# Kernel optimization log

Measured on AMD Instinct MI355X. Metric: run time of the kernel, lower is better.

## Reference

```python
import jax, jax.numpy as jnp
import numpy as np

NUM_LEVELS = 4
RADIUS = 4


def _bilinear_zeros(img, x, y):
    """Bilinear sample img (N,H,W) at absolute pixel coords x,y (N,S,S),
    zeros padding outside, matching torch grid_sample(align_corners=True,
    padding_mode='zeros') with absolute->normalized->absolute roundtrip."""
    N, H, W = img.shape
    x0 = jnp.floor(x); y0 = jnp.floor(y)
    x1 = x0 + 1.0;     y1 = y0 + 1.0
    wx1 = x - x0; wx0 = 1.0 - wx1
    wy1 = y - y0; wy0 = 1.0 - wy1
    flat = img.reshape(N, H * W)

    def gather(xi, yi):
        valid = (xi >= 0) & (xi <= W - 1) & (yi >= 0) & (yi <= H - 1)
        xc = jnp.clip(xi, 0, W - 1).astype(jnp.int32)
        yc = jnp.clip(yi, 0, H - 1).astype(jnp.int32)
        idx = (yc * W + xc).reshape(N, -1)
        v = jnp.take_along_axis(flat, idx, axis=1).reshape(xi.shape)
        return jnp.where(valid, v, jnp.zeros((), img.dtype))

    return (wy0 * wx0 * gather(x0, y0) + wy0 * wx1 * gather(x1, y0)
            + wy1 * wx0 * gather(x0, y1) + wy1 * wx1 * gather(x1, y1))


def _avg_pool2(v):
    N, H, W = v.shape
    return v.reshape(N, H // 2, 2, W // 2, 2).mean(axis=(2, 4))


def setup_inputs() -> dict:
    key = jax.random.key(0)
    k1, k2, k3 = jax.random.split(key, 3)
    B, M, C, H, W = 2, 4096, 256, 64, 64
    fmap1 = jax.random.normal(k1, (B, M, C), dtype=jnp.float32)
    fmap2 = jax.random.normal(k2, (B, C, H, W), dtype=jnp.float32)
    u = jax.random.uniform(k3, (B, M, 2), dtype=jnp.float32)
    centroids_coords = u * jnp.array([W - 1, H - 1], dtype=jnp.float32)
    return {"fmap1": fmap1, "fmap2": fmap2, "centroids_coords": centroids_coords}


def reference(fmap1, fmap2, centroids_coords):
    B, M, C = fmap1.shape
    _, _, H, W = fmap2.shape
    side = 2 * RADIUS + 1

    # correlation volume: (B, M, H, W) -> (B*M, H, W)
    corr = jnp.einsum('bmc,bchw->bmhw', fmap1, fmap2).reshape(B * M, H, W)

    d = jnp.arange(-RADIUS, RADIUS + 1, dtype=centroids_coords.dtype)
    di, dj = jnp.meshgrid(d, d, indexing='ij')
    delta = jnp.stack([di, dj], axis=-1)  # (S, S, 2): ch0 = x-offset, ch1 = y-offset

    c = centroids_coords.reshape(B * M, 1, 1, 2)
    vol = corr
    feats = []
    for lvl in range(NUM_LEVELS):
        sc = c + delta                        # (B*M, S, S, 2)
        sampled = _bilinear_zeros(vol, sc[..., 0], sc[..., 1])
        feats.append(sampled.reshape(B, M, side * side))
        c = c / 2.0
        if lvl < NUM_LEVELS - 1:
            vol = _avg_pool2(vol)
    # (B, M, num_levels*S*S) -> (B, out_channels, M)
    return jnp.concatenate(feats, axis=-1).transpose(0, 2, 1)
```

## Files before the change

### kernel.cpp

```cpp
#include <hip/hip_runtime.h>
#include <stdint.h>
#include <stddef.h>

static constexpr int Bb = 2;
static constexpr int Mq = 4096;
static constexpr int Cc = 256;
static constexpr int Hh = 64, Ww = 64;
static constexpr int Np = Hh * Ww;
static constexpr int NL1 = 1024;
static constexpr int RAD = 4;
static constexpr int SIDE = 2 * RAD + 1;
static constexpr int KPL = SIDE * SIDE;
static constexpr int NLVL = 4;
static constexpr int KTOT = NLVL * KPL;

static constexpr size_t L1BUF_B  = 0;
static constexpr size_t WINBUF_B = (size_t)Bb * Mq * 1024 * 2;
static constexpr size_t ABF_B    = WINBUF_B + (size_t)Bb * Mq * 100 * 4;
static constexpr size_t BT_B     = ABF_B + (size_t)Bb * Mq * Cc * 2;
static constexpr size_t B1T_B    = BT_B + (size_t)Bb * Np * Cc * 2;

typedef float floatx4 __attribute__((ext_vector_type(4)));
typedef short shortx8 __attribute__((ext_vector_type(8)));

union BfPack {
    shortx8 v;
    unsigned short u[8];
};

__device__ __forceinline__ unsigned short f2bf(float f) {
    unsigned int x = __float_as_uint(f);
    x += 0x7fffu + ((x >> 16) & 1u);
    return (unsigned short)(x >> 16);
}

__device__ __forceinline__ float bf2f(unsigned short u) {
    return __uint_as_float((unsigned int)u << 16);
}

__device__ __forceinline__ void gll16(const void* g, void* l) {
    __builtin_amdgcn_global_load_lds(
        (const __attribute__((address_space(1))) unsigned int*)g,
        (__attribute__((address_space(3))) unsigned int*)l, 16, 0, 0);
}

__global__ __launch_bounds__(256)
void cvt_kernel(const float* __restrict__ f1, const float* __restrict__ f2,
                unsigned short* __restrict__ Abf, unsigned short* __restrict__ Bt,
                unsigned short* __restrict__ B1t)
{
    __shared__ float tile[64 * 132];
    const int tid = threadIdx.x;
    if (blockIdx.x < 1024) {
        const int t = blockIdx.x * 256 + tid;
        const float4 v0 = *(const float4*)(f1 + (size_t)t * 8);
        const float4 v1 = *(const float4*)(f1 + (size_t)t * 8 + 4);
        BfPack p;
        p.u[0] = f2bf(v0.x); p.u[1] = f2bf(v0.y);
        p.u[2] = f2bf(v0.z); p.u[3] = f2bf(v0.w);
        p.u[4] = f2bf(v1.x); p.u[5] = f2bf(v1.y);
        p.u[6] = f2bf(v1.z); p.u[7] = f2bf(v1.w);
        *(shortx8*)(Abf + (size_t)t * 8) = p.v;
        return;
    }
    const int bid  = blockIdx.x - 1024;
    const int b    = bid >> 7;
    const int cblk = (bid >> 5) & 3;
    const int y1   = bid & 31;

#pragma unroll
    for (int i = 0; i < 8; ++i) {
        const int v  = i * 256 + tid;
        const int c  = v >> 5;
        const int f4 = v & 31;
        *(float4*)&tile[c * 132 + f4 * 4] =
            *(const float4*)&f2[((size_t)(b * Cc + cblk * 64 + c)) * Np + y1 * 128 + f4 * 4];
    }
    __syncthreads();

#pragma unroll
    for (int i = 0; i < 4; ++i) {
        const int w  = i * 256 + tid;
        const int rp = w >> 3;
        const int cg = w & 7;
        BfPack p;
#pragma unroll
        for (int u = 0; u < 8; ++u)
            p.u[u] = f2bf(tile[(cg * 8 + u) * 132 + rp]);
        *(shortx8*)&Bt[((size_t)(b * Np + y1 * 128 + rp)) * Cc + cblk * 64 + cg * 8] = p.v;
    }

    {
        const int x1 = tid >> 3;
        const int cg = tid & 7;
        BfPack p;
#pragma unroll
        for (int u = 0; u < 8; ++u) {
            const int c = cg * 8 + u;
            const float v = 0.25f * (tile[c * 132 + 2 * x1]      + tile[c * 132 + 2 * x1 + 1]
                                   + tile[c * 132 + 64 + 2 * x1] + tile[c * 132 + 64 + 2 * x1 + 1]);
            p.u[u] = f2bf(v);
        }
        *(shortx8*)&B1t[((size_t)(b * NL1 + y1 * 32 + x1)) * Cc + cblk * 64 + cg * 8] = p.v;
    }
}

__global__ __launch_bounds__(512)
void win_kernel(const unsigned short* __restrict__ Abf,
                const unsigned short* __restrict__ Bt,
                const float* __restrict__ cent,
                float* __restrict__ winbuf)
{
    __shared__ unsigned short reg[176 * 264];
    __shared__ int qlist[128];
    __shared__ int qx0s[128], qy0s[128];
    __shared__ int qcnt;

    const int tid  = threadIdx.x;
    const int b    = blockIdx.x >> 8;
    const int cell = blockIdx.x & 255;
    const int biny = cell >> 4;
    const int binx = cell & 15;
    const int xmin = (4 * binx - 4) > 0 ? (4 * binx - 4) : 0;
    const int ymin = (4 * biny - 4) > 0 ? (4 * biny - 4) : 0;
    const int xmax = (4 * binx + 8) < 63 ? (4 * binx + 8) : 63;
    const int ymax = (4 * biny + 8) < 63 ? (4 * biny + 8) : 63;
    const int rh = ymax - ymin + 1;
    const int rw = xmax - xmin + 1;

    if (tid == 0) qcnt = 0;
    __syncthreads();

#pragma unroll
    for (int i = 0; i < 8; ++i) {
        const int m = i * 512 + tid;
        const float2 cc = *(const float2*)&cent[((size_t)b * Mq + m) * 2];
        const int fx = (int)floorf(cc.x);
        const int fy = (int)floorf(cc.y);
        if ((fx >> 2) == binx && (fy >> 2) == biny) {
            const int idx = atomicAdd(&qcnt, 1);
            if (idx < 128) {
                qlist[idx] = m;
                qx0s[idx] = fx - RAD;
                qy0s[idx] = fy - RAD;
            }
        }
    }

    for (int ry = 0; ry < rh; ++ry) {
        const size_t gbase = ((size_t)(b * Np) + (size_t)((ymin + ry) * Ww + xmin)) * Cc;
        const int nchunk = rw * 32;
        if (tid < nchunk) {
            const int px = tid >> 5;
            const int g  = tid & 31;
            *(shortx8*)&reg[(ry * 13 + px) * 264 + g * 8] =
                *(const shortx8*)&Bt[gbase + (size_t)tid * 8];
        }
    }
    __syncthreads();

    const int cnt = qcnt < 128 ? qcnt : 128;
    const int wave   = tid >> 6;
    const int lane   = tid & 63;
    const int lane15 = lane & 15;
    const int quad   = lane >> 4;

    for (int m0 = 0; m0 < cnt; m0 += 16) {
        const int qidx = (m0 + lane15) < cnt ? (m0 + lane15) : (cnt - 1);
        const unsigned short* arow =
            Abf + (size_t)(b * Mq + qlist[qidx]) * Cc + quad * 8;
        shortx8 afr[8];
#pragma unroll
        for (int k0 = 0; k0 < 8; ++k0)
            afr[k0] = *(const shortx8*)&arow[k0 * 32];

        const int jt0 = wave, jt1 = wave + 8;
        floatx4 acc0 = {0.f, 0.f, 0.f, 0.f};
        floatx4 acc1 = {0.f, 0.f, 0.f, 0.f};
#pragma unroll
        for (int k0 = 0; k0 < 8; ++k0) {
            const shortx8 b0 =
                *(const shortx8*)&reg[(jt0 * 16 + lane15) * 264 + k0 * 32 + quad * 8];
            acc0 = __builtin_amdgcn_mfma_f32_16x16x32_bf16(afr[k0], b0, acc0, 0, 0, 0);
            if (wave < 3) {
                const shortx8 b1 =
                    *(const shortx8*)&reg[(jt1 * 16 + lane15) * 264 + k0 * 32 + quad * 8];
                acc1 = __builtin_amdgcn_mfma_f32_16x16x32_bf16(afr[k0], b1, acc1, 0, 0, 0);
            }
        }

#pragma unroll
        for (int t = 0; t < 2; ++t) {
            if (t == 1 && wave >= 3) break;
            const int jt = (t == 0) ? jt0 : jt1;
            const floatx4 a = (t == 0) ? acc0 : acc1;
            const int col = jt * 16 + lane15;
            const int py = col / 13;
            const int px = col - py * 13;
            if (py < rh && px < rw) {
                const int y = ymin + py, x = xmin + px;
#pragma unroll
                for (int r = 0; r < 4; ++r) {
                    const int qi = m0 + quad * 4 + r;
                    if (qi < cnt) {
                        const int wy = y - qy0s[qi];
                        const int wx = x - qx0s[qi];
                        if ((unsigned)wy < 10u && (unsigned)wx < 10u)
                            winbuf[((size_t)b * Mq + qlist[qi]) * 100 + wy * 10 + wx] = a[r];
                    }
                }
            }
        }
    }
}

__global__ __launch_bounds__(256)
void l1_gemm_kernel(const unsigned short* __restrict__ Abf,
                    const unsigned short* __restrict__ B1t,
                    unsigned short* __restrict__ l1buf)
{
    __shared__ union {
        unsigned short stage[2][2][128 * 32];
        float corrT[32 * 132];
    } sm;

    const int b    = blockIdx.z;
    const int bm0  = blockIdx.y * 128;
    const int bn0  = blockIdx.x * 128;
    const int tid  = threadIdx.x;
    const int lane = tid & 63;
    const int wave = tid >> 6;
    const int lane15 = lane & 15;
    const int quad   = lane >> 4;
    const int wm = (wave >> 1) * 64;
    const int wn = (wave & 1) * 64;

    const int lrow = lane >> 2;
    const int lkg  = (((lane & 3) ^ ((lrow >> 1) & 3))) * 8;
    const unsigned short* aptr = Abf + (size_t)(b * Mq + bm0 + wave * 16 + lrow) * Cc + lkg;
    const unsigned short* bptr = B1t + (size_t)(b * NL1 + bn0 + wave * 16 + lrow) * Cc + lkg;

    floatx4 acc[4][4];
#pragma unroll
    for (int i = 0; i < 4; ++i)
#pragma unroll
        for (int j = 0; j < 4; ++j)
            acc[i][j] = floatx4{0.0f, 0.0f, 0.0f, 0.0f};

    gll16(aptr,           &sm.stage[0][0][wave * 512]);
    gll16(aptr + 64 * Cc, &sm.stage[0][0][2048 + wave * 512]);
    gll16(bptr,           &sm.stage[0][1][wave * 512]);
    gll16(bptr + 64 * Cc, &sm.stage[0][1][2048 + wave * 512]);

    const int rq = (quad ^ ((lane15 >> 1) & 3)) * 8;

    for (int k0 = 0; k0 < 8; ++k0) {
        __syncthreads();
        if (k0 < 7) {
            const int nb = (k0 + 1) & 1;
            const int ko = (k0 + 1) * 32;
            gll16(aptr + ko,           &sm.stage[nb][0][wave * 512]);
            gll16(aptr + 64 * Cc + ko, &sm.stage[nb][0][2048 + wave * 512]);
            gll16(bptr + ko,           &sm.stage[nb][1][wave * 512]);
            gll16(bptr + 64 * Cc + ko, &sm.stage[nb][1][2048 + wave * 512]);
        }
        const unsigned short* la = sm.stage[k0 & 1][0];
        const unsigned short* lb = sm.stage[k0 & 1][1];
        shortx8 af[4], bf[4];
#pragma unroll
        for (int i = 0; i < 4; ++i)
            af[i] = *(const shortx8*)&la[(wm + i * 16 + lane15) * 32 + rq];
#pragma unroll
        for (int j = 0; j < 4; ++j)
            bf[j] = *(const shortx8*)&lb[(wn + j * 16 + lane15) * 32 + rq];
#pragma unroll
        for (int i = 0; i < 4; ++i)
#pragma unroll
            for (int j = 0; j < 4; ++j)
                acc[i][j] = __builtin_amdgcn_mfma_f32_16x16x32_bf16(
                    af[i], bf[j], acc[i][j], 0, 0, 0);
    }

    float* corrT = sm.corrT;
    const int row = tid >> 3;
    const int g   = tid & 7;
#pragma unroll
    for (int c = 0; c < 4; ++c) {
        __syncthreads();
        if ((wave >> 1) == (c >> 1)) {
#pragma unroll
            for (int ii = 0; ii < 2; ++ii) {
                const int i = 2 * (c & 1) + ii;
#pragma unroll
                for (int j = 0; j < 4; ++j) {
#pragma unroll
                    for (int reg = 0; reg < 4; ++reg) {
                        const int rl = ii * 16 + quad * 4 + reg;
                        const int n  = wn + j * 16 + lane15;
                        corrT[rl * 132 + n] = acc[i][j][reg];
                    }
                }
            }
        }
        __syncthreads();

        const size_t gq = (size_t)(b * Mq + bm0 + 32 * c + row);
        const float* T = &corrT[row * 132];
        BfPack p0, p1;
#pragma unroll
        for (int u = 0; u < 8; ++u) {
            p0.u[u] = f2bf(T[g * 16 + u]);
            p1.u[u] = f2bf(T[g * 16 + 8 + u]);
        }
        *(shortx8*)&l1buf[gq * 1024 + bn0 + g * 16]     = p0.v;
        *(shortx8*)&l1buf[gq * 1024 + bn0 + g * 16 + 8] = p1.v;
    }
}

__global__ __launch_bounds__(256)
void pyr_sample_kernel(const float* __restrict__ cent,
                       const unsigned short* __restrict__ l1buf,
                       const float* __restrict__ winbuf,
                       float* __restrict__ out)
{
    __shared__ float l1[8][1024];
    __shared__ float l2[8][256];
    __shared__ float l3[8][64];
    __shared__ float win0[8][100];
    __shared__ float qcx[8], qcy[8];
    __shared__ int   qx0[8], qy0[8];

    const int tid = threadIdx.x;
    const int b   = blockIdx.x >> 9;
    const int m0  = (blockIdx.x & 511) * 8;
    const size_t gq0 = (size_t)(b * Mq + m0);

    if (tid < 8) {
        const float cx = cent[(gq0 + tid) * 2 + 0];
        const float cy = cent[(gq0 + tid) * 2 + 1];
        qcx[tid] = cx; qcy[tid] = cy;
        qx0[tid] = (int)floorf(cx) - RAD;
        qy0[tid] = (int)floorf(cy) - RAD;
    }

#pragma unroll
    for (int it = 0; it < 4; ++it) {
        const int v = it * 256 + tid;
        const int q = v >> 7;
        const int o = v & 127;
        BfPack p;
        p.v = *(const shortx8*)&l1buf[(gq0 + q) * 1024 + o * 8];
#pragma unroll
        for (int u = 0; u < 8; ++u)
            l1[q][o * 8 + u] = bf2f(p.u[u]);
    }
    if (tid < 200) {
        const int q = tid / 25;
        const int o = tid - q * 25;
        *(float4*)&win0[q][o * 4] = *(const float4*)&winbuf[(gq0 + q) * 100 + o * 4];
    }
    __syncthreads();

#pragma unroll
    for (int i = 0; i < 8; ++i) {
        const int idx = i * 256 + tid;
        const int q = idx >> 8;
        const int c = idx & 255;
        const int cy2 = c >> 4, cx2 = c & 15;
        const float* s = &l1[q][(2 * cy2) * 32 + 2 * cx2];
        l2[q][c] = 0.25f * (s[0] + s[1] + s[32] + s[33]);
    }
    __syncthreads();
#pragma unroll
    for (int i = 0; i < 2; ++i) {
        const int idx = i * 256 + tid;
        const int q = idx >> 6;
        const int c = idx & 63;
        const int cy3 = c >> 3, cx3 = c & 7;
        const float* s = &l2[q][(2 * cy3) * 16 + 2 * cx3];
        l3[q][c] = 0.25f * (s[0] + s[1] + s[16] + s[17]);
    }
    __syncthreads();

    for (int i = 0; i < 11; ++i) {
        const int idx = i * 256 + tid;
        if (idx >= KTOT * 8) break;
        const int q  = idx & 7;
        const int kk = idx >> 3;
        const int lvl = kk / KPL;
        const int r   = kk - lvl * KPL;
        const int di  = r / SIDE;
        const int dj  = r - di * SIDE;

        const int w = Ww >> lvl;
        const float scale = 1.0f / (float)(1 << lvl);
        const float x = qcx[q] * scale + (float)(di - RAD);
        const float y = qcy[q] * scale + (float)(dj - RAD);

        const float x0f = floorf(x), y0f = floorf(y);
        const float wx1 = x - x0f, wx0 = 1.0f - wx1;
        const float wy1 = y - y0f, wy0 = 1.0f - wy1;
        const float fmx = (float)(w - 1);
        const bool vx0 = (x0f >= 0.0f) && (x0f <= fmx);
        const bool vx1 = (x0f + 1.0f >= 0.0f) && (x0f + 1.0f <= fmx);
        const bool vy0 = (y0f >= 0.0f) && (y0f <= fmx);
        const bool vy1 = (y0f + 1.0f >= 0.0f) && (y0f + 1.0f <= fmx);

        const int ix0 = (int)x0f, iy0 = (int)y0f;

        const float* buf;
        int stride, ox, oy;
        if (lvl == 0)      { buf = win0[q]; stride = 10; ox = qx0[q]; oy = qy0[q]; }
        else if (lvl == 1) { buf = l1[q];   stride = 32; ox = 0; oy = 0; }
        else if (lvl == 2) { buf = l2[q];   stride = 16; ox = 0; oy = 0; }
        else               { buf = l3[q];   stride =  8; ox = 0; oy = 0; }

        const int cx0 = ix0 - ox, cx1 = ix0 + 1 - ox;
        const int cy0r = iy0 - oy, cy1r = iy0 + 1 - oy;
        const float g00 = (vx0 && vy0) ? buf[cy0r * stride + cx0] : 0.0f;
        const float g10 = (vx1 && vy0) ? buf[cy0r * stride + cx1] : 0.0f;
        const float g01 = (vx0 && vy1) ? buf[cy1r * stride + cx0] : 0.0f;
        const float g11 = (vx1 && vy1) ? buf[cy1r * stride + cx1] : 0.0f;

        out[((size_t)b * KTOT + kk) * Mq + m0 + q] =
            wy0 * (wx0 * g00 + wx1 * g10) + wy1 * (wx0 * g01 + wx1 * g11);
    }
}

extern "C" void kernel_launch(void* const* d_in, const int* in_sizes, int n_in,
                              void* d_out, int out_size, void* d_ws, size_t ws_size,
                              hipStream_t stream)
{
    const float* fmap1 = (const float*)d_in[0];
    const float* fmap2 = (const float*)d_in[1];
    const float* cent  = (const float*)d_in[2];
    char* ws = (char*)d_ws;
    unsigned short* l1buf = (unsigned short*)(ws + L1BUF_B);
    float* winbuf = (float*)(ws + WINBUF_B);
    unsigned short* Abf = (unsigned short*)(ws + ABF_B);
    unsigned short* Bt  = (unsigned short*)(ws + BT_B);
    unsigned short* B1t = (unsigned short*)(ws + B1T_B);
    float* out = (float*)d_out;

    cvt_kernel<<<1280, 256, 0, stream>>>(fmap1, fmap2, Abf, Bt, B1t);

    win_kernel<<<Bb * 256, 512, 0, stream>>>(Abf, Bt, cent, winbuf);

    dim3 ggrid(NL1 / 128, Mq / 128, Bb);
    l1_gemm_kernel<<<ggrid, 256, 0, stream>>>(Abf, B1t, l1buf);

    const int nblk = Bb * Mq / 8;
    pyr_sample_kernel<<<nblk, 256, 0, stream>>>(cent, l1buf, winbuf, out);
}
```

Before: 121.8 us.

## Replace full level-1 correlation GEMM with windowed correlation at every pyramid level

Pools fmap2 down to levels 2 and 3, exploiting the linearity of average pooling and correlation. A single kernel then computes only the 10x10 correlation window each query needs at all four levels, with binned blocks for levels 0 and 1 and per-query blocks for levels 2 and 3. This drops the dense 4096x1024 level-1 GEMM, its bf16 intermediate buffer, and the in-shared pooling in the sampler. The window kernel now reads B tiles straight from global memory instead of staging them in LDS. Pooling the features in bf16 rather than pooling fp32 correlations changes rounding.

```diff
diff --git a/kernel.cpp b/kernel.cpp
--- a/kernel.cpp
+++ b/kernel.cpp
@@ -14,11 +14,12 @@
 static constexpr int NLVL = 4;
 static constexpr int KTOT = NLVL * KPL;
 
-static constexpr size_t L1BUF_B  = 0;
-static constexpr size_t WINBUF_B = (size_t)Bb * Mq * 1024 * 2;
-static constexpr size_t ABF_B    = WINBUF_B + (size_t)Bb * Mq * 100 * 4;
+static constexpr size_t WINBUF_B = 0;
+static constexpr size_t ABF_B    = WINBUF_B + (size_t)Bb * Mq * 400 * 4;
 static constexpr size_t BT_B     = ABF_B + (size_t)Bb * Mq * Cc * 2;
 static constexpr size_t B1T_B    = BT_B + (size_t)Bb * Np * Cc * 2;
+static constexpr size_t B2T_B    = B1T_B + (size_t)Bb * NL1 * Cc * 2;
+static constexpr size_t B3T_B    = B2T_B + (size_t)Bb * 256 * Cc * 2;
 
 typedef float floatx4 __attribute__((ext_vector_type(4)));
 typedef short shortx8 __attribute__((ext_vector_type(8)));
@@ -36,12 +37,6 @@
 
 __device__ __forceinline__ float bf2f(unsigned short u) {
     return __uint_as_float((unsigned int)u << 16);
-}
-
-__device__ __forceinline__ void gll16(const void* g, void* l) {
-    __builtin_amdgcn_global_load_lds(
-        (const __attribute__((address_space(1))) unsigned int*)g,
-        (__attribute__((address_space(3))) unsigned int*)l, 16, 0, 0);
 }
 
 __global__ __launch_bounds__(256)
@@ -105,280 +100,231 @@
     }
 }
 
+__global__ __launch_bounds__(256)
+void pool23_kernel(const unsigned short* __restrict__ B1t,
+                   unsigned short* __restrict__ B2t,
+                   unsigned short* __restrict__ B3t)
+{
+    const int idx = blockIdx.x * 256 + threadIdx.x;
+    if (idx < Bb * 256 * 32) {
+        const int cg = idx & 31;
+        const int p2 = (idx >> 5) & 255;
+        const int b  = idx >> 13;
+        const int y2 = p2 >> 4, x2 = p2 & 15;
+        float s[8] = {0,0,0,0,0,0,0,0};
+#pragma unroll
+        for (int dy = 0; dy < 2; ++dy)
+#pragma unroll
+            for (int dx = 0; dx < 2; ++dx) {
+                const int p1 = (2 * y2 + dy) * 32 + 2 * x2 + dx;
+                BfPack v;
+                v.v = *(const shortx8*)&B1t[((size_t)b * NL1 + p1) * Cc + cg * 8];
+#pragma unroll
+                for (int u = 0; u < 8; ++u) s[u] += bf2f(v.u[u]);
+            }
+        BfPack o;
+#pragma unroll
+        for (int u = 0; u < 8; ++u) o.u[u] = f2bf(0.25f * s[u]);
+        *(shortx8*)&B2t[((size_t)b * 256 + p2) * Cc + cg * 8] = o.v;
+    } else if (idx < Bb * 256 * 32 + Bb * 64 * 32) {
+        const int i = idx - Bb * 256 * 32;
+        const int cg = i & 31;
+        const int p3 = (i >> 5) & 63;
+        const int b  = i >> 11;
+        const int y3 = p3 >> 3, x3 = p3 & 7;
+        float s[8] = {0,0,0,0,0,0,0,0};
+#pragma unroll
+        for (int dy = 0; dy < 4; ++dy)
+#pragma unroll
+            for (int dx = 0; dx < 4; ++dx) {
+                const int p1 = (4 * y3 + dy) * 32 + 4 * x3 + dx;
+                BfPack v;
+                v.v = *(const shortx8*)&B1t[((size_t)b * NL1 + p1) * Cc + cg * 8];
+#pragma unroll
+                for (int u = 0; u < 8; ++u) s[u] += bf2f(v.u[u]);
+            }
+        BfPack o;
+#pragma unroll
+        for (int u = 0; u < 8; ++u) o.u[u] = f2bf(0.0625f * s[u]);
+        *(shortx8*)&B3t[((size_t)b * 64 + p3) * Cc + cg * 8] = o.v;
+    }
+}
+
 __global__ __launch_bounds__(512)
-void win_kernel(const unsigned short* __restrict__ Abf,
-                const unsigned short* __restrict__ Bt,
-                const float* __restrict__ cent,
-                float* __restrict__ winbuf)
-{
-    __shared__ unsigned short reg[176 * 264];
+void win4_kernel(const unsigned short* __restrict__ Abf,
+                 const unsigned short* __restrict__ B0t,
+                 const unsigned short* __restrict__ B1t,
+                 const unsigned short* __restrict__ B2t,
+                 const unsigned short* __restrict__ B3t,
+                 const float* __restrict__ cent,
+                 float* __restrict__ winbuf)
+{
     __shared__ int qlist[128];
     __shared__ int qx0s[128], qy0s[128];
     __shared__ int qcnt;
 
     const int tid  = threadIdx.x;
-    const int b    = blockIdx.x >> 8;
-    const int cell = blockIdx.x & 255;
-    const int biny = cell >> 4;
-    const int binx = cell & 15;
-    const int xmin = (4 * binx - 4) > 0 ? (4 * binx - 4) : 0;
-    const int ymin = (4 * biny - 4) > 0 ? (4 * biny - 4) : 0;
-    const int xmax = (4 * binx + 8) < 63 ? (4 * binx + 8) : 63;
-    const int ymax = (4 * biny + 8) < 63 ? (4 * biny + 8) : 63;
-    const int rh = ymax - ymin + 1;
-    const int rw = xmax - xmin + 1;
-
-    if (tid == 0) qcnt = 0;
-    __syncthreads();
-
-#pragma unroll
-    for (int i = 0; i < 8; ++i) {
-        const int m = i * 512 + tid;
-        const float2 cc = *(const float2*)&cent[((size_t)b * Mq + m) * 2];
-        const int fx = (int)floorf(cc.x);
-        const int fy = (int)floorf(cc.y);
-        if ((fx >> 2) == binx && (fy >> 2) == biny) {
-            const int idx = atomicAdd(&qcnt, 1);
-            if (idx < 128) {
-                qlist[idx] = m;
-                qx0s[idx] = fx - RAD;
-                qy0s[idx] = fy - RAD;
-            }
-        }
-    }
-
-    for (int ry = 0; ry < rh; ++ry) {
-        const size_t gbase = ((size_t)(b * Np) + (size_t)((ymin + ry) * Ww + xmin)) * Cc;
-        const int nchunk = rw * 32;
-        if (tid < nchunk) {
-            const int px = tid >> 5;
-            const int g  = tid & 31;
-            *(shortx8*)&reg[(ry * 13 + px) * 264 + g * 8] =
-                *(const shortx8*)&Bt[gbase + (size_t)tid * 8];
-        }
-    }
-    __syncthreads();
-
-    const int cnt = qcnt < 128 ? qcnt : 128;
-    const int wave   = tid >> 6;
-    const int lane   = tid & 63;
+    const int wave = tid >> 6;
+    const int lane = tid & 63;
     const int lane15 = lane & 15;
     const int quad   = lane >> 4;
+    const int bidx = blockIdx.x;
+
+    int lvl, b, cell = 0, q0 = 0;
+    bool binned;
+    if (bidx < 512)      { lvl = 0; binned = true;  b = bidx >> 8;          cell = bidx & 255; }
+    else if (bidx < 640) { lvl = 1; binned = true;  b = (bidx - 512) >> 6;  cell = (bidx - 512) & 63; }
+    else if (bidx < 768) { lvl = 2; binned = false; b = (bidx - 640) >> 6;  q0 = ((bidx - 640) & 63) * 64; }
+    else                 { lvl = 3; binned = false; b = (bidx - 768) >> 6;  q0 = ((bidx - 768) & 63) * 64; }
+
+    const int w   = Ww >> lvl;
+    const int npx = w * w;
+    const float scale = 1.0f / (float)(1 << lvl);
+    const unsigned short* Bl = (lvl == 0) ? B0t : (lvl == 1) ? B1t : (lvl == 2) ? B2t : B3t;
+
+    int xmin = 0, ymin = 0, rh = w, rw = w, rstride = w, ntile = npx >> 4;
+    int cnt;
+
+    if (binned) {
+        const int ncx  = w >> 2;
+        const int binx = cell & (ncx - 1);
+        const int biny = cell >> (4 - lvl);
+        xmin = 4 * binx - 4; if (xmin < 0) xmin = 0;
+        ymin = 4 * biny - 4; if (ymin < 0) ymin = 0;
+        int xmax = 4 * binx + 8; if (xmax > w - 1) xmax = w - 1;
+        int ymax = 4 * biny + 8; if (ymax > w - 1) ymax = w - 1;
+        rh = ymax - ymin + 1; rw = xmax - xmin + 1;
+        rstride = 13;
+        ntile = (rh * 13 + 15) >> 4;
+
+        if (tid == 0) qcnt = 0;
+        __syncthreads();
+#pragma unroll
+        for (int i = 0; i < 8; ++i) {
+            const int m = i * 512 + tid;
+            const float2 cc = *(const float2*)&cent[((size_t)b * Mq + m) * 2];
+            const int fx = (int)floorf(cc.x * scale);
+            const int fy = (int)floorf(cc.y * scale);
+            if ((fx >> 2) == binx && (fy >> 2) == biny) {
+                const int idx = atomicAdd(&qcnt, 1);
+                if (idx < 128) {
+                    qlist[idx] = m;
+                    qx0s[idx] = fx - RAD;
+                    qy0s[idx] = fy - RAD;
+                }
+            }
+        }
+        __syncthreads();
+        cnt = qcnt < 128 ? qcnt : 128;
+    } else {
+        if (tid < 64) {
+            const int m = q0 + tid;
+            const float2 cc = *(const float2*)&cent[((size_t)b * Mq + m) * 2];
+            qlist[tid] = m;
+            qx0s[tid] = (int)floorf(cc.x * scale) - RAD;
+            qy0s[tid] = (int)floorf(cc.y * scale) - RAD;
+        }
+        __syncthreads();
+        cnt = 64;
+    }
+
+    const int jt0 = wave, jt1 = wave + 8;
+    const bool t0ok = jt0 < ntile;
+    const bool t1ok = jt1 < ntile;
+    int y0 = ymin, x0 = xmin, y1 = ymin, x1 = xmin;
+    bool v0 = false, v1 = false;
+    {
+        const int px = jt0 * 16 + lane15;
+        int py = (rstride == 13) ? ((px * 5043) >> 16) : (px >> (6 - lvl));
+        const int pxx = px - py * rstride;
+        v0 = t0ok && (py < rh) && (pxx < rw);
+        if (py > rh - 1) py = rh - 1;
+        const int pxc = pxx < rw ? pxx : rw - 1;
+        y0 = ymin + py; x0 = xmin + pxc;
+    }
+    {
+        const int px = jt1 * 16 + lane15;
+        int py = (rstride == 13) ? ((px * 5043) >> 16) : (px >> (6 - lvl));
+        const int pxx = px - py * rstride;
+        v1 = t1ok && (py < rh) && (pxx < rw);
+        if (py > rh - 1) py = rh - 1;
+        const int pxc = pxx < rw ? pxx : rw - 1;
+        y1 = ymin + py; x1 = xmin + pxc;
+    }
+    const size_t bB = (size_t)b * npx * Cc;
+    const size_t off0 = bB + (size_t)(y0 * w + x0) * Cc + quad * 8;
+    const size_t off1 = bB + (size_t)(y1 * w + x1) * Cc + quad * 8;
 
     for (int m0 = 0; m0 < cnt; m0 += 16) {
         const int qidx = (m0 + lane15) < cnt ? (m0 + lane15) : (cnt - 1);
-        const unsigned short* arow =
-            Abf + (size_t)(b * Mq + qlist[qidx]) * Cc + quad * 8;
+        const unsigned short* arow = Abf + (size_t)(b * Mq + qlist[qidx]) * Cc + quad * 8;
         shortx8 afr[8];
 #pragma unroll
         for (int k0 = 0; k0 < 8; ++k0)
             afr[k0] = *(const shortx8*)&arow[k0 * 32];
 
-        const int jt0 = wave, jt1 = wave + 8;
         floatx4 acc0 = {0.f, 0.f, 0.f, 0.f};
         floatx4 acc1 = {0.f, 0.f, 0.f, 0.f};
 #pragma unroll
         for (int k0 = 0; k0 < 8; ++k0) {
-            const shortx8 b0 =
-                *(const shortx8*)&reg[(jt0 * 16 + lane15) * 264 + k0 * 32 + quad * 8];
-            acc0 = __builtin_amdgcn_mfma_f32_16x16x32_bf16(afr[k0], b0, acc0, 0, 0, 0);
-            if (wave < 3) {
-                const shortx8 b1 =
-                    *(const shortx8*)&reg[(jt1 * 16 + lane15) * 264 + k0 * 32 + quad * 8];
+            if (t0ok) {
+                const shortx8 b0 = *(const shortx8*)&Bl[off0 + k0 * 32];
+                acc0 = __builtin_amdgcn_mfma_f32_16x16x32_bf16(afr[k0], b0, acc0, 0, 0, 0);
+            }
+            if (t1ok) {
+                const shortx8 b1 = *(const shortx8*)&Bl[off1 + k0 * 32];
                 acc1 = __builtin_amdgcn_mfma_f32_16x16x32_bf16(afr[k0], b1, acc1, 0, 0, 0);
             }
         }
 
 #pragma unroll
         for (int t = 0; t < 2; ++t) {
-            if (t == 1 && wave >= 3) break;
-            const int jt = (t == 0) ? jt0 : jt1;
+            const bool vv = (t == 0) ? v0 : v1;
+            if (!vv) continue;
             const floatx4 a = (t == 0) ? acc0 : acc1;
-            const int col = jt * 16 + lane15;
-            const int py = col / 13;
-            const int px = col - py * 13;
-            if (py < rh && px < rw) {
-                const int y = ymin + py, x = xmin + px;
-#pragma unroll
-                for (int r = 0; r < 4; ++r) {
-                    const int qi = m0 + quad * 4 + r;
-                    if (qi < cnt) {
-                        const int wy = y - qy0s[qi];
-                        const int wx = x - qx0s[qi];
-                        if ((unsigned)wy < 10u && (unsigned)wx < 10u)
-                            winbuf[((size_t)b * Mq + qlist[qi]) * 100 + wy * 10 + wx] = a[r];
-                    }
+            const int yy = (t == 0) ? y0 : y1;
+            const int xx = (t == 0) ? x0 : x1;
+#pragma unroll
+            for (int r = 0; r < 4; ++r) {
+                const int qi = m0 + quad * 4 + r;
+                if (qi < cnt) {
+                    const int wy = yy - qy0s[qi];
+                    const int wx = xx - qx0s[qi];
+                    if ((unsigned)wy < 10u && (unsigned)wx < 10u)
+                        winbuf[((size_t)b * Mq + qlist[qi]) * 400 + lvl * 100 + wy * 10 + wx] = a[r];
                 }
             }
         }
-    }
-}
-
-__global__ __launch_bounds__(256)
-void l1_gemm_kernel(const unsigned short* __restrict__ Abf,
-                    const unsigned short* __restrict__ B1t,
-                    unsigned short* __restrict__ l1buf)
-{
-    __shared__ union {
-        unsigned short stage[2][2][128 * 32];
-        float corrT[32 * 132];
-    } sm;
-
-    const int b    = blockIdx.z;
-    const int bm0  = blockIdx.y * 128;
-    const int bn0  = blockIdx.x * 128;
-    const int tid  = threadIdx.x;
-    const int lane = tid & 63;
-    const int wave = tid >> 6;
-    const int lane15 = lane & 15;
-    const int quad   = lane >> 4;
-    const int wm = (wave >> 1) * 64;
-    const int wn = (wave & 1) * 64;
-
-    const int lrow = lane >> 2;
-    const int lkg  = (((lane & 3) ^ ((lrow >> 1) & 3))) * 8;
-    const unsigned short* aptr = Abf + (size_t)(b * Mq + bm0 + wave * 16 + lrow) * Cc + lkg;
-    const unsigned short* bptr = B1t + (size_t)(b * NL1 + bn0 + wave * 16 + lrow) * Cc + lkg;
-
-    floatx4 acc[4][4];
-#pragma unroll
-    for (int i = 0; i < 4; ++i)
-#pragma unroll
-        for (int j = 0; j < 4; ++j)
-            acc[i][j] = floatx4{0.0f, 0.0f, 0.0f, 0.0f};
-
-    gll16(aptr,           &sm.stage[0][0][wave * 512]);
-    gll16(aptr + 64 * Cc, &sm.stage[0][0][2048 + wave * 512]);
-    gll16(bptr,           &sm.stage[0][1][wave * 512]);
-    gll16(bptr + 64 * Cc, &sm.stage[0][1][2048 + wave * 512]);
-
-    const int rq = (quad ^ ((lane15 >> 1) & 3)) * 8;
-
-    for (int k0 = 0; k0 < 8; ++k0) {
-        __syncthreads();
-        if (k0 < 7) {
-            const int nb = (k0 + 1) & 1;
-            const int ko = (k0 + 1) * 32;
-            gll16(aptr + ko,           &sm.stage[nb][0][wave * 512]);
-            gll16(aptr + 64 * Cc + ko, &sm.stage[nb][0][2048 + wave * 512]);
-            gll16(bptr + ko,           &sm.stage[nb][1][wave * 512]);
-            gll16(bptr + 64 * Cc + ko, &sm.stage[nb][1][2048 + wave * 512]);
-        }
-        const unsigned short* la = sm.stage[k0 & 1][0];
-        const unsigned short* lb = sm.stage[k0 & 1][1];
-        shortx8 af[4], bf[4];
-#pragma unroll
-        for (int i = 0; i < 4; ++i)
-            af[i] = *(const shortx8*)&la[(wm + i * 16 + lane15) * 32 + rq];
-#pragma unroll
-        for (int j = 0; j < 4; ++j)
-            bf[j] = *(const shortx8*)&lb[(wn + j * 16 + lane15) * 32 + rq];
-#pragma unroll
-        for (int i = 0; i < 4; ++i)
-#pragma unroll
-            for (int j = 0; j < 4; ++j)
-                acc[i][j] = __builtin_amdgcn_mfma_f32_16x16x32_bf16(
-                    af[i], bf[j], acc[i][j], 0, 0, 0);
-    }
-
-    float* corrT = sm.corrT;
-    const int row = tid >> 3;
-    const int g   = tid & 7;
-#pragma unroll
-    for (int c = 0; c < 4; ++c) {
-        __syncthreads();
-        if ((wave >> 1) == (c >> 1)) {
-#pragma unroll
-            for (int ii = 0; ii < 2; ++ii) {
-                const int i = 2 * (c & 1) + ii;
-#pragma unroll
-                for (int j = 0; j < 4; ++j) {
-#pragma unroll
-                    for (int reg = 0; reg < 4; ++reg) {
-                        const int rl = ii * 16 + quad * 4 + reg;
-                        const int n  = wn + j * 16 + lane15;
-                        corrT[rl * 132 + n] = acc[i][j][reg];
-                    }
-                }
-            }
-        }
-        __syncthreads();
-
-        const size_t gq = (size_t)(b * Mq + bm0 + 32 * c + row);
-        const float* T = &corrT[row * 132];
-        BfPack p0, p1;
-#pragma unroll
-        for (int u = 0; u < 8; ++u) {
-            p0.u[u] = f2bf(T[g * 16 + u]);
-            p1.u[u] = f2bf(T[g * 16 + 8 + u]);
-        }
-        *(shortx8*)&l1buf[gq * 1024 + bn0 + g * 16]     = p0.v;
-        *(shortx8*)&l1buf[gq * 1024 + bn0 + g * 16 + 8] = p1.v;
     }
 }
 
 __global__ __launch_bounds__(256)
 void pyr_sample_kernel(const float* __restrict__ cent,
-                       const unsigned short* __restrict__ l1buf,
                        const float* __restrict__ winbuf,
                        float* __restrict__ out)
 {
-    __shared__ float l1[8][1024];
-    __shared__ float l2[8][256];
-    __shared__ float l3[8][64];
-    __shared__ float win0[8][100];
+    __shared__ float win[8][400];
     __shared__ float qcx[8], qcy[8];
-    __shared__ int   qx0[8], qy0[8];
+    __shared__ int qx0l[8][4], qy0l[8][4];
 
     const int tid = threadIdx.x;
     const int b   = blockIdx.x >> 9;
     const int m0  = (blockIdx.x & 511) * 8;
     const size_t gq0 = (size_t)(b * Mq + m0);
 
-    if (tid < 8) {
-        const float cx = cent[(gq0 + tid) * 2 + 0];
-        const float cy = cent[(gq0 + tid) * 2 + 1];
-        qcx[tid] = cx; qcy[tid] = cy;
-        qx0[tid] = (int)floorf(cx) - RAD;
-        qy0[tid] = (int)floorf(cy) - RAD;
-    }
-
-#pragma unroll
-    for (int it = 0; it < 4; ++it) {
-        const int v = it * 256 + tid;
-        const int q = v >> 7;
-        const int o = v & 127;
-        BfPack p;
-        p.v = *(const shortx8*)&l1buf[(gq0 + q) * 1024 + o * 8];
-#pragma unroll
-        for (int u = 0; u < 8; ++u)
-            l1[q][o * 8 + u] = bf2f(p.u[u]);
-    }
-    if (tid < 200) {
-        const int q = tid / 25;
-        const int o = tid - q * 25;
-        *(float4*)&win0[q][o * 4] = *(const float4*)&winbuf[(gq0 + q) * 100 + o * 4];
-    }
-    __syncthreads();
-
-#pragma unroll
-    for (int i = 0; i < 8; ++i) {
-        const int idx = i * 256 + tid;
-        const int q = idx >> 8;
-        const int c = idx & 255;
-        const int cy2 = c >> 4, cx2 = c & 15;
-        const float* s = &l1[q][(2 * cy2) * 32 + 2 * cx2];
-        l2[q][c] = 0.25f * (s[0] + s[1] + s[32] + s[33]);
-    }
-    __syncthreads();
-#pragma unroll
-    for (int i = 0; i < 2; ++i) {
-        const int idx = i * 256 + tid;
-        const int q = idx >> 6;
-        const int c = idx & 63;
-        const int cy3 = c >> 3, cx3 = c & 7;
-        const float* s = &l2[q][(2 * cy3) * 16 + 2 * cx3];
-        l3[q][c] = 0.25f * (s[0] + s[1] + s[16] + s[17]);
+    if (tid < 32) {
+        const int q = tid >> 2, l = tid & 3;
+        const float cx = cent[(gq0 + q) * 2 + 0];
+        const float cy = cent[(gq0 + q) * 2 + 1];
+        if (l == 0) { qcx[q] = cx; qcy[q] = cy; }
+        const float scl = 1.0f / (float)(1 << l);
+        qx0l[q][l] = (int)floorf(cx * scl) - RAD;
+        qy0l[q][l] = (int)floorf(cy * scl) - RAD;
+    }
+    for (int v = tid; v < 800; v += 256) {
+        const int q = (v * 41) >> 12;
+        const int o = v - q * 100;
+        *(float4*)&win[q][o * 4] = *(const float4*)&winbuf[(gq0 + q) * 400 + o * 4];
     }
     __syncthreads();
 
@@ -408,19 +354,14 @@
 
         const int ix0 = (int)x0f, iy0 = (int)y0f;
 
-        const float* buf;
-        int stride, ox, oy;
-        if (lvl == 0)      { buf = win0[q]; stride = 10; ox = qx0[q]; oy = qy0[q]; }
-        else if (lvl == 1) { buf = l1[q];   stride = 32; ox = 0; oy = 0; }
-        else if (lvl == 2) { buf = l2[q];   stride = 16; ox = 0; oy = 0; }
-        else               { buf = l3[q];   stride =  8; ox = 0; oy = 0; }
-
-        const int cx0 = ix0 - ox, cx1 = ix0 + 1 - ox;
-        const int cy0r = iy0 - oy, cy1r = iy0 + 1 - oy;
-        const float g00 = (vx0 && vy0) ? buf[cy0r * stride + cx0] : 0.0f;
-        const float g10 = (vx1 && vy0) ? buf[cy0r * stride + cx1] : 0.0f;
-        const float g01 = (vx0 && vy1) ? buf[cy1r * stride + cx0] : 0.0f;
-        const float g11 = (vx1 && vy1) ? buf[cy1r * stride + cx1] : 0.0f;
+        const float* buf = &win[q][lvl * 100];
+        const int ox = qx0l[q][lvl], oy = qy0l[q][lvl];
+        const int cx0 = ix0 - ox, cx1 = cx0 + 1;
+        const int cy0r = iy0 - oy, cy1r = cy0r + 1;
+        const float g00 = (vx0 && vy0) ? buf[cy0r * 10 + cx0] : 0.0f;
+        const float g10 = (vx1 && vy0) ? buf[cy0r * 10 + cx1] : 0.0f;
+        const float g01 = (vx0 && vy1) ? buf[cy1r * 10 + cx0] : 0.0f;
+        const float g11 = (vx1 && vy1) ? buf[cy1r * 10 + cx1] : 0.0f;
 
         out[((size_t)b * KTOT + kk) * Mq + m0 + q] =
             wy0 * (wx0 * g00 + wx1 * g10) + wy1 * (wx0 * g01 + wx1 * g11);
@@ -435,20 +376,19 @@
     const float* fmap2 = (const float*)d_in[1];
     const float* cent  = (const float*)d_in[2];
     char* ws = (char*)d_ws;
-    unsigned short* l1buf = (unsigned short*)(ws + L1BUF_B);
     float* winbuf = (float*)(ws + WINBUF_B);
     unsigned short* Abf = (unsigned short*)(ws + ABF_B);
     unsigned short* Bt  = (unsigned short*)(ws + BT_B);
     unsigned short* B1t = (unsigned short*)(ws + B1T_B);
+    unsigned short* B2t = (unsigned short*)(ws + B2T_B);
+    unsigned short* B3t = (unsigned short*)(ws + B3T_B);
     float* out = (float*)d_out;
 
     cvt_kernel<<<1280, 256, 0, stream>>>(fmap1, fmap2, Abf, Bt, B1t);
 
-    win_kernel<<<Bb * 256, 512, 0, stream>>>(Abf, Bt, cent, winbuf);
-
-    dim3 ggrid(NL1 / 128, Mq / 128, Bb);
-    l1_gemm_kernel<<<ggrid, 256, 0, stream>>>(Abf, B1t, l1buf);
-
-    const int nblk = Bb * Mq / 8;
-    pyr_sample_kernel<<<nblk, 256, 0, stream>>>(cent, l1buf, winbuf, out);
-}
+    pool23_kernel<<<80, 256, 0, stream>>>(B1t, B2t, B3t);
+
+    win4_kernel<<<896, 512, 0, stream>>>(Abf, Bt, B1t, B2t, B3t, cent, winbuf);
+
+    pyr_sample_kernel<<<Bb * Mq / 8, 256, 0, stream>>>(cent, winbuf, out);
+}
```

New measurement: 144.8 us. +18.9%, slower.
